# Performance work log

Measured on AMD Instinct MI355X. Metric: run time of the kernel, lower is better.

Reference implementation:

```python
import jax, jax.numpy as jnp
import numpy as np

N, E = 50000, 800000
IN_C, OUT_C, D_EMB = 64, 64, 64
NEG_SLOPE = 0.2  # GDN GraphLayer default leaky_relu slope


def setup_inputs() -> dict:
    key = jax.random.key(0)
    ks = jax.random.split(key, 9)
    return {
        "x": jax.random.normal(ks[0], (N, IN_C), jnp.float32),
        "edge_index": jax.random.randint(ks[1], (2, E), 0, N, dtype=jnp.int32),
        "embedding": jax.random.normal(ks[2], (N, D_EMB), jnp.float32),
        # learned params of GraphLayer (heads=1, concat)
        "W": jax.random.normal(ks[3], (OUT_C, IN_C), jnp.float32) * (1.0 / np.sqrt(IN_C)),
        "att_i": jax.random.normal(ks[4], (OUT_C,), jnp.float32) * 0.1,
        "att_j": jax.random.normal(ks[5], (OUT_C,), jnp.float32) * 0.1,
        "att_em_i": jax.random.normal(ks[6], (D_EMB,), jnp.float32) * 0.1,
        "att_em_j": jax.random.normal(ks[7], (D_EMB,), jnp.float32) * 0.1,
        "bias": jax.random.normal(ks[8], (OUT_C,), jnp.float32) * 0.01,
    }


def reference(x, edge_index, embedding, W, att_i, att_j, att_em_i, att_em_j, bias):
    n = x.shape[0]
    loops = jnp.arange(n, dtype=edge_index.dtype)
    src = jnp.concatenate([edge_index[0], loops])  # message source j
    dst = jnp.concatenate([edge_index[1], loops])  # message target i

    h = x @ W.T  # [N, OUT_C]
    # per-node attention scores (equivalent to cat(h, emb) . cat(att, att_em))
    s_i = h @ att_i + embedding @ att_em_i  # [N]
    s_j = h @ att_j + embedding @ att_em_j  # [N]

    alpha = s_i[dst] + s_j[src]                         # [E+N] edge logits
    alpha = jax.nn.leaky_relu(alpha, NEG_SLOPE)
    # softmax over incoming edges of each destination node
    amax = jax.ops.segment_max(alpha, dst, num_segments=n)
    ex = jnp.exp(alpha - amax[dst])
    denom = jax.ops.segment_sum(ex, dst, num_segments=n)
    alpha = ex / (denom[dst] + 1e-16)

    msg = h[src] * alpha[:, None]                       # [E+N, OUT_C]
    out = jax.ops.segment_sum(msg, dst, num_segments=n) + bias
    return jax.nn.relu(out)
```

## Files before the change

### kernel.cpp

```cpp
#include <hip/hip_runtime.h>
#include <hip/hip_bf16.h>
#include <math.h>

#define NEG_SLOPE 0.2f

#define XTA(k, r) ((k) * 132 + ((r) ^ ((((k) >> 2) & 7) << 2)))

__global__ __launch_bounds__(256) void k_gemm(
    const float* __restrict__ x, const float* __restrict__ emb,
    const float* __restrict__ W,
    const float* __restrict__ att_i, const float* __restrict__ att_j,
    const float* __restrict__ att_em_i, const float* __restrict__ att_em_j,
    __hip_bfloat16* __restrict__ h, float* __restrict__ s_i,
    float* __restrict__ s_j, int N)
{
    __shared__ float lds[13056];
    const int tid = threadIdx.x;

    float* XT = lds;
    float* WT = lds + 8704;

    const int rbase = blockIdx.x * 128;
    const int valid = min(128, N - rbase);

    #pragma unroll
    for (int i = 0; i < 8; ++i) {
        int idx = i * 256 + tid;
        int r = idx >> 4, m = idx & 15;
        float4 v = make_float4(0.f, 0.f, 0.f, 0.f);
        if (r < valid)
            v = *reinterpret_cast<const float4*>(x + (size_t)(rbase + r) * 64 + 4 * m);
        int k = 4 * m;
        XT[XTA(k + 0, r)] = v.x;
        XT[XTA(k + 1, r)] = v.y;
        XT[XTA(k + 2, r)] = v.z;
        XT[XTA(k + 3, r)] = v.w;
    }
    #pragma unroll
    for (int i = 0; i < 16; ++i) {
        int idx = i * 256 + tid;
        int c = idx >> 6, k = idx & 63;
        WT[k * 68 + c] = W[idx];
    }
    __syncthreads();

    const int cg = tid & 15, rg = tid >> 4;
    const int c0 = cg * 4, r0 = rg * 8;
    float acc[4][8];
    #pragma unroll
    for (int a = 0; a < 4; ++a)
        #pragma unroll
        for (int b = 0; b < 8; ++b) acc[a][b] = 0.f;

    #pragma unroll 4
    for (int k = 0; k < 64; ++k) {
        float4 wv = *reinterpret_cast<float4*>(&WT[k * 68 + c0]);
        float4 xa = *reinterpret_cast<float4*>(&XT[XTA(k, r0)]);
        float4 xb = *reinterpret_cast<float4*>(&XT[XTA(k, r0 + 4)]);
        float xs[8] = {xa.x, xa.y, xa.z, xa.w, xb.x, xb.y, xb.z, xb.w};
        float ws[4] = {wv.x, wv.y, wv.z, wv.w};
        #pragma unroll
        for (int a = 0; a < 4; ++a)
            #pragma unroll
            for (int b = 0; b < 8; ++b)
                acc[a][b] = fmaf(ws[a], xs[b], acc[a][b]);
    }

    #pragma unroll
    for (int b = 0; b < 8; ++b) {
        int r = r0 + b;
        if (r < valid) {
            union { __hip_bfloat16 q[4]; uint2 u; } pk;
            pk.q[0] = __float2bfloat16(acc[0][b]);
            pk.q[1] = __float2bfloat16(acc[1][b]);
            pk.q[2] = __float2bfloat16(acc[2][b]);
            pk.q[3] = __float2bfloat16(acc[3][b]);
            *reinterpret_cast<uint2*>(h + (size_t)(rbase + r) * 64 + c0) = pk.u;
        }
    }

    float ai[4], aj[4];
    #pragma unroll
    for (int a = 0; a < 4; ++a) { ai[a] = att_i[c0 + a]; aj[a] = att_j[c0 + a]; }

    __syncthreads();
    float* EMT   = lds;
    float* RED_I = lds + 8704;
    float* RED_J = lds + 8704 + 2176;

    #pragma unroll
    for (int b = 0; b < 8; ++b) {
        int r = r0 + b;
        float pi = acc[0][b]*ai[0] + acc[1][b]*ai[1] + acc[2][b]*ai[2] + acc[3][b]*ai[3];
        float pj = acc[0][b]*aj[0] + acc[1][b]*aj[1] + acc[2][b]*aj[2] + acc[3][b]*aj[3];
        RED_I[r * 17 + cg] = pi;
        RED_J[r * 17 + cg] = pj;
    }
    #pragma unroll
    for (int i = 0; i < 8; ++i) {
        int idx = i * 256 + tid;
        int r = idx >> 4, m = idx & 15;
        float4 v = make_float4(0.f, 0.f, 0.f, 0.f);
        if (r < valid)
            v = *reinterpret_cast<const float4*>(emb + (size_t)(rbase + r) * 64 + 4 * m);
        int k = 4 * m;
        EMT[(k + 0) * 131 + r] = v.x;
        EMT[(k + 1) * 131 + r] = v.y;
        EMT[(k + 2) * 131 + r] = v.z;
        EMT[(k + 3) * 131 + r] = v.w;
    }
    __syncthreads();

    if (tid < 128 && tid < valid) {
        float ri = 0.f, rj = 0.f;
        #pragma unroll
        for (int j = 0; j < 16; ++j) {
            ri += RED_I[tid * 17 + j];
            rj += RED_J[tid * 17 + j];
        }
        float ei = 0.f, ej = 0.f;
        #pragma unroll 16
        for (int k = 0; k < 64; ++k) {
            float ev = EMT[k * 131 + tid];
            ei = fmaf(ev, att_em_i[k], ei);
            ej = fmaf(ev, att_em_j[k], ej);
        }
        s_i[rbase + tid] = ri + ei;
        s_j[rbase + tid] = rj + ej;
    }
}

__global__ __launch_bounds__(256) void k_scatter_bkt(
    const int* __restrict__ srcA, const int* __restrict__ dstA,
    int* __restrict__ cursor, unsigned short* __restrict__ csr,
    int E, int sh, int nchunks)
{
    const int oct   = blockIdx.x & 7;
    const int chunk = blockIdx.x >> 3;
    const int stride = nchunks * 256;

    for (int e = chunk * 256 + threadIdx.x; e < E; e += stride) {
        int d = dstA[e];
        if ((d >> sh) == oct) {
            int pos = atomicAdd(&cursor[d], 1);
            if (pos < 64)
                csr[(size_t)d * 64 + pos] = (unsigned short)srcA[e];
        }
    }
}

__global__ __launch_bounds__(256) void k_aggregate(
    const __hip_bfloat16* __restrict__ h, const float* __restrict__ s_i,
    const float* __restrict__ s_j, const int* __restrict__ cursor,
    const unsigned short* __restrict__ csr, const float* __restrict__ bias,
    float* __restrict__ out, int N)
{
    const int lane = threadIdx.x & 63;
    const int node = (blockIdx.x * blockDim.x + threadIdx.x) >> 6;
    if (node >= N) return;

    int deg_e = cursor[node];
    deg_e = (deg_e > 63) ? 63 : deg_e;
    const int degT = deg_e + 1;
    const float si = s_i[node];

    int s = node;
    if (lane < deg_e) s = csr[(size_t)node * 64 + lane];
    float a = -INFINITY;
    if (lane < degT) {
        a = si + s_j[s];
        a = (a > 0.f) ? a : NEG_SLOPE * a;
    }
    float m = a;
    #pragma unroll
    for (int off = 32; off > 0; off >>= 1) m = fmaxf(m, __shfl_xor(m, off));
    float ex = (lane < degT) ? __expf(a - m) : 0.f;
    float l = ex;
    #pragma unroll
    for (int off = 32; off > 0; off >>= 1) l += __shfl_xor(l, off);

    const int half = lane >> 5;
    const int hc   = lane & 31;
    const unsigned* hp = reinterpret_cast<const unsigned*>(h);
    float ax = 0.f, ay = 0.f;

    int j = 0;
    for (; j + 4 <= degT; j += 4) {
        int j0 = j + half, j1 = j + 2 + half;
        float e0 = __shfl(ex, j0), e1 = __shfl(ex, j1);
        int   t0 = __shfl(s, j0),  t1 = __shfl(s, j1);
        unsigned u0 = hp[(size_t)t0 * 32 + hc];
        unsigned u1 = hp[(size_t)t1 * 32 + hc];
        float lo0 = __uint_as_float(u0 << 16);
        float hi0 = __uint_as_float(u0 & 0xffff0000u);
        float lo1 = __uint_as_float(u1 << 16);
        float hi1 = __uint_as_float(u1 & 0xffff0000u);
        ax = fmaf(e0, lo0, ax); ay = fmaf(e0, hi0, ay);
        ax = fmaf(e1, lo1, ax); ay = fmaf(e1, hi1, ay);
    }
    for (; j < degT; j += 2) {
        int jj = j + half;
        int jc = (jj < degT) ? jj : (degT - 1);
        float e = __shfl(ex, jc);
        int   t = __shfl(s, jc);
        if (jj >= degT) e = 0.f;
        unsigned u = hp[(size_t)t * 32 + hc];
        ax = fmaf(e, __uint_as_float(u << 16), ax);
        ay = fmaf(e, __uint_as_float(u & 0xffff0000u), ay);
    }

    ax += __shfl_xor(ax, 32);
    ay += __shfl_xor(ay, 32);

    if (half == 0) {
        float inv = 1.f / (l + 1e-16f);
        float2 bv = *reinterpret_cast<const float2*>(bias + 2 * hc);
        float2 o;
        o.x = fmaxf(ax * inv + bv.x, 0.f);
        o.y = fmaxf(ay * inv + bv.y, 0.f);
        *reinterpret_cast<float2*>(out + (size_t)node * 64 + 2 * hc) = o;
    }
}

extern "C" void kernel_launch(void* const* d_in, const int* in_sizes, int n_in,
                              void* d_out, int out_size, void* d_ws, size_t ws_size,
                              hipStream_t stream) {
    const float* x        = (const float*)d_in[0];
    const int*   ei       = (const int*)  d_in[1];
    const float* emb      = (const float*)d_in[2];
    const float* W        = (const float*)d_in[3];
    const float* att_i    = (const float*)d_in[4];
    const float* att_j    = (const float*)d_in[5];
    const float* att_em_i = (const float*)d_in[6];
    const float* att_em_j = (const float*)d_in[7];
    const float* bias     = (const float*)d_in[8];
    float* out = (float*)d_out;

    const int N = in_sizes[0] / 64;
    const int E = in_sizes[1] / 2;
    const int* e_src = ei;
    const int* e_dst = ei + E;

    char* ws = (char*)d_ws;
    __hip_bfloat16* h = (__hip_bfloat16*)ws;  ws += (size_t)N * 64 * 2;
    float* s_i     = (float*)ws;  ws += (size_t)N * 4;
    float* s_j     = (float*)ws;  ws += (size_t)N * 4;
    int*   cursor  = (int*)ws;    ws += (size_t)N * 4;
    unsigned short* csr = (unsigned short*)ws;  ws += (size_t)N * 64 * 2;

    int sh = 0;
    while ((1 << sh) < N) ++sh;
    sh -= 3;

    const int GB = (N + 127) / 128;
    const int NCHUNK = 512;

    hipMemsetAsync(cursor, 0, (size_t)N * 4, stream);
    k_gemm<<<GB, 256, 0, stream>>>(x, emb, W, att_i, att_j, att_em_i,
                                   att_em_j, h, s_i, s_j, N);
    k_scatter_bkt<<<NCHUNK * 8, 256, 0, stream>>>(e_src, e_dst, cursor, csr,
                                                  E, sh, NCHUNK);
    k_aggregate<<<(N * 64 + 255) / 256, 256, 0, stream>>>(h, s_i, s_j, cursor,
                                                          csr, bias, out, N);
}
```

Baseline: 170.9 us.

## Fuse GEMM and edge-bucket scatter into one heterogeneous launch

Merges the projection GEMM kernel and the CSR scatter kernel into a single launch, where the first GB blocks do the GEMM and the remaining blocks do the atomic edge bucketing. The two independent stages can then overlap on the GPU and one launch gap is removed. The GEMM tile shrinks from 128 to 64 rows, which cuts LDS use and allows more resident blocks, and W is now loaded with float4 reads. The scatter uses fewer chunks (128 instead of 512), so each scatter block loops over more edges.

```diff
diff --git a/kernel.cpp b/kernel.cpp
--- a/kernel.cpp
+++ b/kernel.cpp
@@ -4,27 +4,45 @@
 
 #define NEG_SLOPE 0.2f
 
-#define XTA(k, r) ((k) * 132 + ((r) ^ ((((k) >> 2) & 7) << 2)))
-
-__global__ __launch_bounds__(256) void k_gemm(
+#define XTA(k, r) ((k) * 68 + ((r) ^ ((((k) >> 2) & 7) << 2)))
+
+__global__ __launch_bounds__(256) void k_gemm_scatter(
     const float* __restrict__ x, const float* __restrict__ emb,
     const float* __restrict__ W,
     const float* __restrict__ att_i, const float* __restrict__ att_j,
     const float* __restrict__ att_em_i, const float* __restrict__ att_em_j,
+    const int* __restrict__ srcA, const int* __restrict__ dstA,
+    int* __restrict__ cursor, unsigned short* __restrict__ csr,
     __hip_bfloat16* __restrict__ h, float* __restrict__ s_i,
-    float* __restrict__ s_j, int N)
+    float* __restrict__ s_j, int N, int E, int GB, int sh, int nchunks)
 {
-    __shared__ float lds[13056];
+    __shared__ float lds[8704];
     const int tid = threadIdx.x;
 
+    if ((int)blockIdx.x >= GB) {
+        int b     = blockIdx.x - GB;
+        int oct   = b & 7;
+        int chunk = b >> 3;
+        int stride = nchunks * 256;
+        for (int e = chunk * 256 + tid; e < E; e += stride) {
+            int d = dstA[e];
+            if ((d >> sh) == oct) {
+                int pos = atomicAdd(&cursor[d], 1);
+                if (pos < 64)
+                    csr[(size_t)d * 64 + pos] = (unsigned short)srcA[e];
+            }
+        }
+        return;
+    }
+
     float* XT = lds;
-    float* WT = lds + 8704;
-
-    const int rbase = blockIdx.x * 128;
-    const int valid = min(128, N - rbase);
-
-    #pragma unroll
-    for (int i = 0; i < 8; ++i) {
+    float* WT = lds + 4352;
+
+    const int rbase = blockIdx.x * 64;
+    const int valid = min(64, N - rbase);
+
+    #pragma unroll
+    for (int i = 0; i < 4; ++i) {
         int idx = i * 256 + tid;
         int r = idx >> 4, m = idx & 15;
         float4 v = make_float4(0.f, 0.f, 0.f, 0.f);
@@ -37,37 +55,41 @@
         XT[XTA(k + 3, r)] = v.w;
     }
     #pragma unroll
-    for (int i = 0; i < 16; ++i) {
+    for (int i = 0; i < 4; ++i) {
         int idx = i * 256 + tid;
-        int c = idx >> 6, k = idx & 63;
-        WT[k * 68 + c] = W[idx];
+        int c = idx >> 4, m = idx & 15;
+        float4 v = *reinterpret_cast<const float4*>(W + idx * 4);
+        int k = 4 * m;
+        WT[(k + 0) * 68 + c] = v.x;
+        WT[(k + 1) * 68 + c] = v.y;
+        WT[(k + 2) * 68 + c] = v.z;
+        WT[(k + 3) * 68 + c] = v.w;
     }
     __syncthreads();
 
     const int cg = tid & 15, rg = tid >> 4;
-    const int c0 = cg * 4, r0 = rg * 8;
-    float acc[4][8];
+    const int c0 = cg * 4, r0 = rg * 4;
+    float acc[4][4];
     #pragma unroll
     for (int a = 0; a < 4; ++a)
         #pragma unroll
-        for (int b = 0; b < 8; ++b) acc[a][b] = 0.f;
+        for (int b = 0; b < 4; ++b) acc[a][b] = 0.f;
 
     #pragma unroll 4
     for (int k = 0; k < 64; ++k) {
         float4 wv = *reinterpret_cast<float4*>(&WT[k * 68 + c0]);
         float4 xa = *reinterpret_cast<float4*>(&XT[XTA(k, r0)]);
-        float4 xb = *reinterpret_cast<float4*>(&XT[XTA(k, r0 + 4)]);
-        float xs[8] = {xa.x, xa.y, xa.z, xa.w, xb.x, xb.y, xb.z, xb.w};
+        float xs[4] = {xa.x, xa.y, xa.z, xa.w};
         float ws[4] = {wv.x, wv.y, wv.z, wv.w};
         #pragma unroll
         for (int a = 0; a < 4; ++a)
             #pragma unroll
-            for (int b = 0; b < 8; ++b)
+            for (int b = 0; b < 4; ++b)
                 acc[a][b] = fmaf(ws[a], xs[b], acc[a][b]);
     }
 
     #pragma unroll
-    for (int b = 0; b < 8; ++b) {
+    for (int b = 0; b < 4; ++b) {
         int r = r0 + b;
         if (r < valid) {
             union { __hip_bfloat16 q[4]; uint2 u; } pk;
@@ -84,12 +106,12 @@
     for (int a = 0; a < 4; ++a) { ai[a] = att_i[c0 + a]; aj[a] = att_j[c0 + a]; }
 
     __syncthreads();
-    float* EMT   = lds;
-    float* RED_I = lds + 8704;
-    float* RED_J = lds + 8704 + 2176;
-
-    #pragma unroll
-    for (int b = 0; b < 8; ++b) {
+    float* RED_I = lds;
+    float* RED_J = lds + 1088;
+    float* EMT   = lds + 4352;
+
+    #pragma unroll
+    for (int b = 0; b < 4; ++b) {
         int r = r0 + b;
         float pi = acc[0][b]*ai[0] + acc[1][b]*ai[1] + acc[2][b]*ai[2] + acc[3][b]*ai[3];
         float pj = acc[0][b]*aj[0] + acc[1][b]*aj[1] + acc[2][b]*aj[2] + acc[3][b]*aj[3];
@@ -97,21 +119,21 @@
         RED_J[r * 17 + cg] = pj;
     }
     #pragma unroll
-    for (int i = 0; i < 8; ++i) {
+    for (int i = 0; i < 4; ++i) {
         int idx = i * 256 + tid;
         int r = idx >> 4, m = idx & 15;
         float4 v = make_float4(0.f, 0.f, 0.f, 0.f);
         if (r < valid)
             v = *reinterpret_cast<const float4*>(emb + (size_t)(rbase + r) * 64 + 4 * m);
         int k = 4 * m;
-        EMT[(k + 0) * 131 + r] = v.x;
-        EMT[(k + 1) * 131 + r] = v.y;
-        EMT[(k + 2) * 131 + r] = v.z;
-        EMT[(k + 3) * 131 + r] = v.w;
+        EMT[(k + 0) * 67 + r] = v.x;
+        EMT[(k + 1) * 67 + r] = v.y;
+        EMT[(k + 2) * 67 + r] = v.z;
+        EMT[(k + 3) * 67 + r] = v.w;
     }
     __syncthreads();
 
-    if (tid < 128 && tid < valid) {
+    if (tid < 64 && tid < valid) {
         float ri = 0.f, rj = 0.f;
         #pragma unroll
         for (int j = 0; j < 16; ++j) {
@@ -121,31 +143,12 @@
         float ei = 0.f, ej = 0.f;
         #pragma unroll 16
         for (int k = 0; k < 64; ++k) {
-            float ev = EMT[k * 131 + tid];
+            float ev = EMT[k * 67 + tid];
             ei = fmaf(ev, att_em_i[k], ei);
             ej = fmaf(ev, att_em_j[k], ej);
         }
         s_i[rbase + tid] = ri + ei;
         s_j[rbase + tid] = rj + ej;
-    }
-}
-
-__global__ __launch_bounds__(256) void k_scatter_bkt(
-    const int* __restrict__ srcA, const int* __restrict__ dstA,
-    int* __restrict__ cursor, unsigned short* __restrict__ csr,
-    int E, int sh, int nchunks)
-{
-    const int oct   = blockIdx.x & 7;
-    const int chunk = blockIdx.x >> 3;
-    const int stride = nchunks * 256;
-
-    for (int e = chunk * 256 + threadIdx.x; e < E; e += stride) {
-        int d = dstA[e];
-        if ((d >> sh) == oct) {
-            int pos = atomicAdd(&cursor[d], 1);
-            if (pos < 64)
-                csr[(size_t)d * 64 + pos] = (unsigned short)srcA[e];
-        }
     }
 }
 
@@ -252,14 +255,13 @@
     while ((1 << sh) < N) ++sh;
     sh -= 3;
 
-    const int GB = (N + 127) / 128;
-    const int NCHUNK = 512;
+    const int GB = (N + 63) / 64;
+    const int NCHUNK = 128;
 
     hipMemsetAsync(cursor, 0, (size_t)N * 4, stream);
-    k_gemm<<<GB, 256, 0, stream>>>(x, emb, W, att_i, att_j, att_em_i,
-                                   att_em_j, h, s_i, s_j, N);
-    k_scatter_bkt<<<NCHUNK * 8, 256, 0, stream>>>(e_src, e_dst, cursor, csr,
-                                                  E, sh, NCHUNK);
+    k_gemm_scatter<<<GB + NCHUNK * 8, 256, 0, stream>>>(
+        x, emb, W, att_i, att_j, att_em_i, att_em_j,
+        e_src, e_dst, cursor, csr, h, s_i, s_j, N, E, GB, sh, NCHUNK);
     k_aggregate<<<(N * 64 + 255) / 256, 256, 0, stream>>>(h, s_i, s_j, cursor,
                                                           csr, bias, out, N);
 }
```

After: 164.1 us. 1.04x faster.
